# Kernel optimization log

Hardware: AMD Instinct MI355X
Metric: run time of the kernel (lower is better)

Reference implementation:

```python
import jax, jax.numpy as jnp
import numpy as np

EPS = 1e-5
N_HEAD = 12
N_LAYER = 12
D = 768
VOCAB = 50257
SEQ = 1024


def layer_norm(x, w, b):
    m = jnp.mean(x, axis=-1, keepdims=True)
    v = jnp.mean(jnp.square(x - m), axis=-1, keepdims=True)
    return (x - m) * jax.lax.rsqrt(v + EPS) * w + b


def setup_inputs() -> dict:
    key = jax.random.key(0)
    ks = jax.random.split(key, 8)
    s = 0.02  # gpt2 init scale
    return {
        "input_ids": jax.random.randint(ks[0], (SEQ,), 0, VOCAB, dtype=jnp.int64 if jax.config.jax_enable_x64 else jnp.int32),
        "wte": jax.random.normal(ks[1], (VOCAB, D), jnp.float32) * s,
        "wpe": jax.random.normal(ks[2], (SEQ, D), jnp.float32) * s,
        "ln1_w": jnp.ones((N_LAYER, D), jnp.float32),
        "ln1_b": jnp.zeros((N_LAYER, D), jnp.float32),
        "qkv_w": jax.random.normal(ks[3], (N_LAYER, D, 3 * D), jnp.float32) * s,
        "qkv_b": jnp.zeros((N_LAYER, 3 * D), jnp.float32),
        "out_w": jax.random.normal(ks[4], (N_LAYER, D, D), jnp.float32) * s,
        "out_b": jnp.zeros((N_LAYER, D), jnp.float32),
        "ln2_w": jnp.ones((N_LAYER, D), jnp.float32),
        "ln2_b": jnp.zeros((N_LAYER, D), jnp.float32),
        "up_w": jax.random.normal(ks[5], (N_LAYER, D, 4 * D), jnp.float32) * s,
        "up_b": jnp.zeros((N_LAYER, 4 * D), jnp.float32),
        "down_w": jax.random.normal(ks[6], (N_LAYER, 4 * D, D), jnp.float32) * s,
        "down_b": jnp.zeros((N_LAYER, D), jnp.float32),
        "lnf_w": jnp.ones((D,), jnp.float32),
        "lnf_b": jnp.zeros((D,), jnp.float32),
    }


def _attention(x, qkv_w, qkv_b, out_w, out_b, causal_mask):
    S = x.shape[0]
    d = D // N_HEAD
    qkv = x @ qkv_w + qkv_b                  # [S, 3D]
    q, k, v = jnp.split(qkv, 3, axis=-1)     # each [S, D]
    q = q.reshape(S, N_HEAD, d)
    k = k.reshape(S, N_HEAD, d)
    v = v.reshape(S, N_HEAD, d)
    scores = jnp.einsum('shd,thd->hst', q, k) / np.sqrt(d).astype(np.float32)
    scores = jnp.where(causal_mask, scores, jnp.finfo(scores.dtype).min)
    p = jax.nn.softmax(scores, axis=-1)      # [H, S, S]
    o = jnp.einsum('hst,thd->shd', p, v).reshape(S, D)
    return o @ out_w + out_b


def reference(input_ids, wte, wpe, ln1_w, ln1_b, qkv_w, qkv_b, out_w, out_b,
              ln2_w, ln2_b, up_w, up_b, down_w, down_b, lnf_w, lnf_b):
    S = input_ids.shape[0]
    h0 = wte[input_ids] + wpe[jnp.arange(S)]        # [S, D]
    causal_mask = jnp.tril(jnp.ones((S, S), bool))

    layer_params = (ln1_w, ln1_b, qkv_w, qkv_b, out_w, out_b,
                    ln2_w, ln2_b, up_w, up_b, down_w, down_b)

    def step(x, p):
        l1w, l1b, qw, qb, ow, ob, l2w, l2b, uw, ub, dw, db = p
        x = x + _attention(layer_norm(x, l1w, l1b), qw, qb, ow, ob, causal_mask)
        x = x + (jax.nn.gelu(layer_norm(x, l2w, l2b) @ uw + ub, approximate=True) @ dw + db)
        return x, x

    h, ys = jax.lax.scan(step, h0, layer_params)
    layers_output = jnp.concatenate([h0[None], ys], axis=0)   # [L+1, S, D]
    return layer_norm(h, lnf_w, lnf_b), layers_output
```

## Files before the change

kernel.cpp:

```cpp
#include <hip/hip_runtime.h>

typedef __bf16 bf16_t;
typedef __bf16 bf16x8 __attribute__((ext_vector_type(8)));
typedef __bf16 bf16x4 __attribute__((ext_vector_type(4)));
typedef float f32x4 __attribute__((ext_vector_type(4)));

#define MFMA16(a, b, c) __builtin_amdgcn_mfma_f32_16x16x32_bf16(a, b, c, 0, 0, 0)

__device__ __forceinline__ f32x4 zero4() {
    f32x4 z = {0.f, 0.f, 0.f, 0.f};
    return z;
}

__device__ __forceinline__ float gelu_f(float v) {
    float u = 0.7978845608028654f * (v + 0.044715f * v * v * v);
    float e = __expf(2.0f * u);
    float th = 1.0f - 2.0f / (e + 1.0f);
    return 0.5f * v * (1.0f + th);
}

__device__ __forceinline__ void gload16(const bf16_t* g, bf16_t* l) {
    __builtin_amdgcn_global_load_lds((const __attribute__((address_space(1))) void*)g,
                                     (__attribute__((address_space(3))) void*)l, 16, 0, 0);
}

__global__ __launch_bounds__(256) void embed_kernel(const int* __restrict__ ids,
                                                    const float* __restrict__ wte,
                                                    const float* __restrict__ wpe,
                                                    float* __restrict__ x,
                                                    float* __restrict__ out0) {
    const int s = blockIdx.x;
    const int id = ids[s];
    const size_t base = (size_t)s * 768;
#pragma unroll
    for (int r = 0; r < 3; ++r) {
        int d = threadIdx.x + r * 256;
        float v = wte[(size_t)id * 768 + d] + wpe[base + d];
        x[base + d] = v;
        out0[base + d] = v;
    }
}

template <bool BF16OUT>
__global__ __launch_bounds__(256) void ln_kernel(const float* __restrict__ x,
                                                 const float* __restrict__ w,
                                                 const float* __restrict__ b,
                                                 void* __restrict__ outp) {
    const int row = blockIdx.x;
    const int t = threadIdx.x;
    const float* xr = x + (size_t)row * 768;
    float v0 = xr[t], v1 = xr[t + 256], v2 = xr[t + 512];
    float s = v0 + v1 + v2;
    float q = v0 * v0 + v1 * v1 + v2 * v2;
#pragma unroll
    for (int off = 32; off >= 1; off >>= 1) {
        s += __shfl_xor(s, off);
        q += __shfl_xor(q, off);
    }
    __shared__ float sh_s[4], sh_q[4];
    if ((t & 63) == 0) {
        sh_s[t >> 6] = s;
        sh_q[t >> 6] = q;
    }
    __syncthreads();
    s = sh_s[0] + sh_s[1] + sh_s[2] + sh_s[3];
    q = sh_q[0] + sh_q[1] + sh_q[2] + sh_q[3];
    const float mean = s * (1.0f / 768.0f);
    const float var = q * (1.0f / 768.0f) - mean * mean;
    const float rstd = rsqrtf(var + 1e-5f);
    float vv[3] = {v0, v1, v2};
#pragma unroll
    for (int r = 0; r < 3; ++r) {
        int d = t + r * 256;
        float y = (vv[r] - mean) * rstd * w[d] + b[d];
        if (BF16OUT)
            ((bf16_t*)outp)[(size_t)row * 768 + d] = (bf16_t)y;
        else
            ((float*)outp)[(size_t)row * 768 + d] = y;
    }
}

template <bool FINAL>
__global__ __launch_bounds__(256) void ln_reduce(const float* __restrict__ p0,
                                                 const float* __restrict__ p1,
                                                 const float* __restrict__ db,
                                                 float* __restrict__ x,
                                                 float* __restrict__ slice,
                                                 void* __restrict__ lnout,
                                                 const float* __restrict__ w,
                                                 const float* __restrict__ b) {
    const int row = blockIdx.x;
    const int t = threadIdx.x;
    const size_t base = (size_t)row * 768;
    float vv[3];
#pragma unroll
    for (int r = 0; r < 3; ++r) {
        int d = t + r * 256;
        float v = x[base + d] + p0[base + d] + p1[base + d] + db[d];
        vv[r] = v;
        x[base + d] = v;
        slice[base + d] = v;
    }
    float s = vv[0] + vv[1] + vv[2];
    float q = vv[0] * vv[0] + vv[1] * vv[1] + vv[2] * vv[2];
#pragma unroll
    for (int off = 32; off >= 1; off >>= 1) {
        s += __shfl_xor(s, off);
        q += __shfl_xor(q, off);
    }
    __shared__ float sh_s[4], sh_q[4];
    if ((t & 63) == 0) {
        sh_s[t >> 6] = s;
        sh_q[t >> 6] = q;
    }
    __syncthreads();
    s = sh_s[0] + sh_s[1] + sh_s[2] + sh_s[3];
    q = sh_q[0] + sh_q[1] + sh_q[2] + sh_q[3];
    const float mean = s * (1.0f / 768.0f);
    const float var = q * (1.0f / 768.0f) - mean * mean;
    const float rstd = rsqrtf(var + 1e-5f);
#pragma unroll
    for (int r = 0; r < 3; ++r) {
        int d = t + r * 256;
        float y = (vv[r] - mean) * rstd * w[d] + b[d];
        if (FINAL)
            ((float*)lnout)[base + d] = y;
        else
            ((bf16_t*)lnout)[base + d] = (bf16_t)y;
    }
}

__global__ __launch_bounds__(256) void transpose_cvt(const float* __restrict__ src0,
                                                     bf16_t* __restrict__ dst0, int K, int N) {
    const int l = blockIdx.z;
    const float* src = src0 + (size_t)l * K * N;
    bf16_t* dst = dst0 + (size_t)l * N * K;
    const int n0 = blockIdx.x * 32;
    const int k0 = blockIdx.y * 32;
    __shared__ float tile[32][36];
    const int t = threadIdx.x;
    const int r = t >> 3, c4 = (t & 7) * 4;
    const float4 v = *(const float4*)&src[(size_t)(k0 + r) * N + n0 + c4];
    tile[r][c4 + 0] = v.x;
    tile[r][c4 + 1] = v.y;
    tile[r][c4 + 2] = v.z;
    tile[r][c4 + 3] = v.w;
    __syncthreads();
    bf16x4 o;
    o[0] = (bf16_t)tile[c4 + 0][r];
    o[1] = (bf16_t)tile[c4 + 1][r];
    o[2] = (bf16_t)tile[c4 + 2][r];
    o[3] = (bf16_t)tile[c4 + 3][r];
    *(bf16x4*)&dst[(size_t)(n0 + r) * K + k0 + c4] = o;
}

template <int BM, int BN, bool GELU, bool RES>
__global__ __launch_bounds__(256) void gemm3(const bf16_t* __restrict__ A,
                                             const bf16_t* __restrict__ BT,
                                             const float* __restrict__ bias,
                                             const float* __restrict__ res,
                                             float* __restrict__ outF,
                                             bf16_t* __restrict__ outB, int N, int LDK,
                                             int KLEN) {
    constexpr int MW = BM / 32, NW = BN / 32;
    constexpr int TILE = (BM + BN) * 64;
    constexpr int LOADS = (BM + BN) / 32;
    __shared__ __align__(16) bf16_t lds[3 * TILE];
    const int tid = threadIdx.x;
    const int lane = tid & 63, wv = tid >> 6, wm = wv >> 1, wn = wv & 1;
    const int lr = lane & 15, lg = lane >> 4;
    const int m0 = blockIdx.x * BM, n0 = blockIdx.y * BN;
    const bf16_t* Ap = A + (size_t)m0 * LDK + (size_t)blockIdx.z * KLEN;
    const bf16_t* Bp = BT + (size_t)n0 * LDK + (size_t)blockIdx.z * KLEN;

    f32x4 acc[MW][NW];
#pragma unroll
    for (int i = 0; i < MW; ++i)
#pragma unroll
        for (int j = 0; j < NW; ++j) acc[i][j] = zero4();

    const int KT = KLEN >> 6;

    auto stage = [&](int buf, int kt) {
        bf16_t* Ad = lds + buf * TILE;
        bf16_t* Bd = Ad + BM * 64;
#pragma unroll
        for (int i = 0; i < BM / 32; ++i) {
            int v = i * 256 + tid;
            int row = v >> 3, cg = v & 7;
            gload16(Ap + (size_t)row * LDK + kt * 64 + ((cg ^ (row & 7)) << 3), Ad + v * 8);
        }
#pragma unroll
        for (int i = 0; i < BN / 32; ++i) {
            int v = i * 256 + tid;
            int row = v >> 3, cg = v & 7;
            gload16(Bp + (size_t)row * LDK + kt * 64 + ((cg ^ (row & 7)) << 3), Bd + v * 8);
        }
    };

    stage(0, 0);
    stage(1, 1);
    int buf = 0;
    for (int kt = 0; kt < KT; ++kt) {
        if (kt + 1 < KT) {
            if constexpr (LOADS == 4)
                asm volatile("s_waitcnt vmcnt(4)" ::: "memory");
            else
                asm volatile("s_waitcnt vmcnt(3)" ::: "memory");
        } else {
            asm volatile("s_waitcnt vmcnt(0)" ::: "memory");
        }
        __builtin_amdgcn_s_barrier();
        if (kt + 2 < KT) stage((kt + 2) % 3, kt + 2);
        const bf16_t* Ab = lds + buf * TILE;
        const bf16_t* Bb = Ab + BM * 64;
#pragma unroll
        for (int c = 0; c < 2; ++c) {
            bf16x8 af[MW], bfr[NW];
#pragma unroll
            for (int i = 0; i < MW; ++i) {
                int row = wm * (BM / 2) + i * 16 + lr;
                af[i] = *(const bf16x8*)&Ab[row * 64 + ((c * 32 + lg * 8) ^ ((row & 7) << 3))];
            }
#pragma unroll
            for (int j = 0; j < NW; ++j) {
                int row = wn * (BN / 2) + j * 16 + lr;
                bfr[j] = *(const bf16x8*)&Bb[row * 64 + ((c * 32 + lg * 8) ^ ((row & 7) << 3))];
            }
#pragma unroll
            for (int i = 0; i < MW; ++i)
#pragma unroll
                for (int j = 0; j < NW; ++j) acc[i][j] = MFMA16(af[i], bfr[j], acc[i][j]);
        }
        buf = (buf + 1) % 3;
    }

    float* o1 = outF ? outF + (size_t)blockIdx.z * ((size_t)1024 * N) : nullptr;
#pragma unroll
    for (int i = 0; i < MW; ++i) {
#pragma unroll
        for (int j = 0; j < NW; ++j) {
            const int col = n0 + wn * (BN / 2) + j * 16 + lr;
            const float bc = bias ? bias[col] : 0.f;
#pragma unroll
            for (int ii = 0; ii < 4; ++ii) {
                const int rrow = m0 + wm * (BM / 2) + i * 16 + lg * 4 + ii;
                float v = acc[i][j][ii] + bc;
                if (GELU) v = gelu_f(v);
                if (RES) v += res[(size_t)rrow * N + col];
                if (o1) o1[(size_t)rrow * N + col] = v;
                if (outB) outB[(size_t)rrow * N + col] = (bf16_t)v;
            }
        }
    }
}

__global__ __launch_bounds__(256) void attn3_kernel(const bf16_t* __restrict__ qkv,
                                                    bf16_t* __restrict__ out) {
    const int qb = 31 - blockIdx.x;
    const int h = blockIdx.y;
    const int tid = threadIdx.x;
    const int w = tid >> 6, lane = tid & 63;
    const int lr = lane & 15, lg = lane >> 4;
    const int qsub = w & 1, ks = w >> 1;
    const int q0 = qb * 32;
    const int qr0 = q0 + qsub * 16;
    const int NT = (q0 >> 6) + 1;

    __shared__ bf16_t Ksh[2][64][72];
    __shared__ bf16_t Vsh[2][64][72];
    __shared__ bf16_t Ps[4][16][72];
    __shared__ float Osh[2][16][64];
    __shared__ float mlsh[2][2][16];

    bf16x8 aq[2];
    {
        const size_t qoff = (size_t)(qr0 + lr) * 2304 + h * 64;
#pragma unroll
        for (int dt = 0; dt < 2; ++dt) {
            bf16x8 v = *(const bf16x8*)&qkv[qoff + dt * 32 + lg * 8];
#pragma unroll
            for (int i = 0; i < 8; ++i) v[i] = (bf16_t)((float)v[i] * 0.125f);
            aq[dt] = v;
        }
    }

    f32x4 oacc[4];
#pragma unroll
    for (int i = 0; i < 4; ++i) oacc[i] = zero4();
    float mrun[4], lrun[4];
#pragma unroll
    for (int i = 0; i < 4; ++i) {
        mrun[i] = -3.0e38f;
        lrun[i] = 0.f;
    }

    const int st = tid >> 7;
    const int srow = (tid >> 1) & 63;
    const int rounds = (NT + 1) >> 1;

    for (int rr = 0; rr < rounds; ++rr) {
        const int skb = 2 * rr + st;
        if (skb < NT) {
            const int k0s = skb * 64;
#pragma unroll
            for (int s2 = 0; s2 < 2; ++s2) {
                const int dbase = (tid & 1) * 32 + s2 * 16;
                const size_t roff = (size_t)(k0s + srow) * 2304 + h * 64 + dbase;
                bf16x8 ka = *(const bf16x8*)&qkv[roff + 768];
                bf16x8 kbv = *(const bf16x8*)&qkv[roff + 768 + 8];
                bf16x8 va = *(const bf16x8*)&qkv[roff + 1536];
                bf16x8 vb = *(const bf16x8*)&qkv[roff + 1536 + 8];
                *(bf16x8*)&Ksh[st][srow][dbase] = ka;
                *(bf16x8*)&Ksh[st][srow][dbase + 8] = kbv;
#pragma unroll
                for (int i = 0; i < 8; ++i) {
                    Vsh[st][dbase + i][srow] = va[i];
                    Vsh[st][dbase + 8 + i][srow] = vb[i];
                }
            }
        }
        __syncthreads();

        const int kb = 2 * rr + ks;
        if (kb < NT) {
            const int k0 = kb * 64;
            f32x4 sacc[4];
#pragma unroll
            for (int i = 0; i < 4; ++i) sacc[i] = zero4();
#pragma unroll
            for (int kt = 0; kt < 4; ++kt)
#pragma unroll
                for (int dt = 0; dt < 2; ++dt) {
                    bf16x8 bk = *(const bf16x8*)&Ksh[ks][kt * 16 + lr][dt * 32 + lg * 8];
                    sacc[kt] = MFMA16(aq[dt], bk, sacc[kt]);
                }

            if (kb == NT - 1) {
#pragma unroll
                for (int kt = 0; kt < 4; ++kt)
#pragma unroll
                    for (int i = 0; i < 4; ++i)
                        if (k0 + kt * 16 + lr > qr0 + lg * 4 + i) sacc[kt][i] = -3.0e38f;
            }

#pragma unroll
            for (int i = 0; i < 4; ++i) {
                float rmax = fmaxf(fmaxf(sacc[0][i], sacc[1][i]), fmaxf(sacc[2][i], sacc[3][i]));
                rmax = fmaxf(rmax, __shfl_xor(rmax, 1));
                rmax = fmaxf(rmax, __shfl_xor(rmax, 2));
                rmax = fmaxf(rmax, __shfl_xor(rmax, 4));
                rmax = fmaxf(rmax, __shfl_xor(rmax, 8));
                const float mnew = fmaxf(mrun[i], rmax);
                const float sf = __expf(mrun[i] - mnew);
                mrun[i] = mnew;
                float rsum = 0.f;
#pragma unroll
                for (int kt = 0; kt < 4; ++kt) {
                    float p = __expf(sacc[kt][i] - mnew);
                    rsum += p;
                    Ps[w][lg * 4 + i][kt * 16 + lr] = (bf16_t)p;
                }
                rsum += __shfl_xor(rsum, 1);
                rsum += __shfl_xor(rsum, 2);
                rsum += __shfl_xor(rsum, 4);
                rsum += __shfl_xor(rsum, 8);
                lrun[i] = lrun[i] * sf + rsum;
#pragma unroll
                for (int ot = 0; ot < 4; ++ot) oacc[ot][i] *= sf;
            }

            bf16x8 pa0 = *(const bf16x8*)&Ps[w][lr][lg * 8];
            bf16x8 pa1 = *(const bf16x8*)&Ps[w][lr][32 + lg * 8];
#pragma unroll
            for (int ot = 0; ot < 4; ++ot) {
                bf16x8 bv0 = *(const bf16x8*)&Vsh[ks][ot * 16 + lr][lg * 8];
                bf16x8 bv1 = *(const bf16x8*)&Vsh[ks][ot * 16 + lr][32 + lg * 8];
                oacc[ot] = MFMA16(pa0, bv0, oacc[ot]);
                oacc[ot] = MFMA16(pa1, bv1, oacc[ot]);
            }
        }
        __syncthreads();
    }

    if (ks == 1) {
        if (lr == 0) {
#pragma unroll
            for (int i = 0; i < 4; ++i) {
                mlsh[qsub][0][lg * 4 + i] = mrun[i];
                mlsh[qsub][1][lg * 4 + i] = lrun[i];
            }
        }
#pragma unroll
        for (int ot = 0; ot < 4; ++ot)
#pragma unroll
            for (int i = 0; i < 4; ++i) Osh[qsub][lg * 4 + i][ot * 16 + lr] = oacc[ot][i];
    }
    __syncthreads();
    if (ks == 0) {
#pragma unroll
        for (int ot = 0; ot < 4; ++ot)
#pragma unroll
            for (int i = 0; i < 4; ++i) {
                const int row = lg * 4 + i;
                const float m1 = mlsh[qsub][0][row], l1 = mlsh[qsub][1][row];
                const float mm = fmaxf(mrun[i], m1);
                const float fa = __expf(mrun[i] - mm), fb = __expf(m1 - mm);
                const float ll = lrun[i] * fa + l1 * fb;
                const float v = (oacc[ot][i] * fa + Osh[qsub][row][ot * 16 + lr] * fb) / ll;
                out[(size_t)(qr0 + row) * 768 + h * 64 + ot * 16 + lr] = (bf16_t)v;
            }
    }
}

extern "C" void kernel_launch(void* const* d_in, const int* in_sizes, int n_in, void* d_out,
                              int out_size, void* d_ws, size_t ws_size, hipStream_t stream) {
    const int* ids = (const int*)d_in[0];
    const float* wte = (const float*)d_in[1];
    const float* wpe = (const float*)d_in[2];
    const float* ln1_w = (const float*)d_in[3];
    const float* ln1_b = (const float*)d_in[4];
    const float* qkv_w = (const float*)d_in[5];
    const float* qkv_b = (const float*)d_in[6];
    const float* out_w = (const float*)d_in[7];
    const float* out_b = (const float*)d_in[8];
    const float* ln2_w = (const float*)d_in[9];
    const float* ln2_b = (const float*)d_in[10];
    const float* up_w = (const float*)d_in[11];
    const float* up_b = (const float*)d_in[12];
    const float* down_w = (const float*)d_in[13];
    const float* down_b = (const float*)d_in[14];
    const float* lnf_w = (const float*)d_in[15];
    const float* lnf_b = (const float*)d_in[16];

    char* ws = (char*)d_ws;
    float* x = (float*)(ws + 0);
    bf16_t* a_bf = (bf16_t*)(ws + 3145728);
    bf16_t* qkv_bf = (bf16_t*)(ws + 4718592);
    bf16_t* attn_bf = (bf16_t*)(ws + 9437184);
    bf16_t* u_bf = (bf16_t*)(ws + 11010048);
    float* p0 = (float*)(ws + 4718592);
    float* p1 = (float*)(ws + 7864320);
    bf16_t* wqkv_t = (bf16_t*)(ws + 17301504);
    bf16_t* wout_t = (bf16_t*)(ws + 59768832);
    bf16_t* wup_t = (bf16_t*)(ws + 73924608);
    bf16_t* wdown_t = (bf16_t*)(ws + 130547712);

    float* outF = (float*)d_out;
    const size_t SD = (size_t)1024 * 768;
    float* out_layers = outF + SD;

    transpose_cvt<<<dim3(72, 24, 12), 256, 0, stream>>>(qkv_w, wqkv_t, 768, 2304);
    transpose_cvt<<<dim3(24, 24, 12), 256, 0, stream>>>(out_w, wout_t, 768, 768);
    transpose_cvt<<<dim3(96, 24, 12), 256, 0, stream>>>(up_w, wup_t, 768, 3072);
    transpose_cvt<<<dim3(24, 96, 12), 256, 0, stream>>>(down_w, wdown_t, 3072, 768);

    embed_kernel<<<1024, 256, 0, stream>>>(ids, wte, wpe, x, out_layers);

    for (int l = 0; l < 12; ++l) {
        const size_t l768 = (size_t)l * 768;
        if (l == 0)
            ln_kernel<true><<<1024, 256, 0, stream>>>(x, ln1_w, ln1_b, a_bf);
        else
            ln_reduce<false><<<1024, 256, 0, stream>>>(p0, p1, down_b + (l - 1) * 768, x,
                                                       out_layers + (size_t)l * SD, a_bf,
                                                       ln1_w + l768, ln1_b + l768);
        gemm3<64, 64, false, false><<<dim3(16, 36), 256, 0, stream>>>(
            a_bf, wqkv_t + (size_t)l * 2304 * 768, qkv_b + (size_t)l * 2304, nullptr, nullptr,
            qkv_bf, 2304, 768, 768);
        attn3_kernel<<<dim3(32, 12), 256, 0, stream>>>(qkv_bf, attn_bf);
        gemm3<32, 64, false, true><<<dim3(32, 12), 256, 0, stream>>>(
            attn_bf, wout_t + (size_t)l * 768 * 768, out_b + l768, x, x, nullptr, 768, 768,
            768);
        ln_kernel<true><<<1024, 256, 0, stream>>>(x, ln2_w + l768, ln2_b + l768, a_bf);
        gemm3<64, 64, true, false><<<dim3(16, 48), 256, 0, stream>>>(
            a_bf, wup_t + (size_t)l * 3072 * 768, up_b + (size_t)l * 3072, nullptr, nullptr,
            u_bf, 3072, 768, 768);
        gemm3<32, 64, false, false><<<dim3(32, 12, 2), 256, 0, stream>>>(
            u_bf, wdown_t + (size_t)l * 768 * 3072, nullptr, nullptr, p0, nullptr, 768, 3072,
            1536);
    }
    ln_reduce<true><<<1024, 256, 0, stream>>>(p0, p1, down_b + 11 * 768, x,
                                              out_layers + 12 * SD, outF, lnf_w, lnf_b);
}
```

Before: 1.117 ms.

## Emit transposed V from QKV GEMM and async-load swizzled K/V tiles in attention

Measured after the change: 1.085 ms. -2.8%, faster.

```diff
diff --git a/kernel.cpp b/kernel.cpp
--- a/kernel.cpp
+++ b/kernel.cpp
@@ -154,13 +154,14 @@
     *(bf16x4*)&dst[(size_t)(n0 + r) * K + k0 + c4] = o;
 }
 
-template <int BM, int BN, bool GELU, bool RES>
+template <int BM, int BN, bool GELU, bool RES, bool VT>
 __global__ __launch_bounds__(256) void gemm3(const bf16_t* __restrict__ A,
                                              const bf16_t* __restrict__ BT,
                                              const float* __restrict__ bias,
                                              const float* __restrict__ res,
                                              float* __restrict__ outF,
-                                             bf16_t* __restrict__ outB, int N, int LDK,
+                                             bf16_t* __restrict__ outB,
+                                             bf16_t* __restrict__ vt, int N, int LDK,
                                              int KLEN) {
     constexpr int MW = BM / 32, NW = BN / 32;
     constexpr int TILE = (BM + BN) * 64;
@@ -242,6 +243,7 @@
         for (int j = 0; j < NW; ++j) {
             const int col = n0 + wn * (BN / 2) + j * 16 + lr;
             const float bc = bias ? bias[col] : 0.f;
+            float vr[4];
 #pragma unroll
             for (int ii = 0; ii < 4; ++ii) {
                 const int rrow = m0 + wm * (BM / 2) + i * 16 + lg * 4 + ii;
@@ -250,12 +252,21 @@
                 if (RES) v += res[(size_t)rrow * N + col];
                 if (o1) o1[(size_t)rrow * N + col] = v;
                 if (outB) outB[(size_t)rrow * N + col] = (bf16_t)v;
-            }
-        }
-    }
-}
-
-__global__ __launch_bounds__(256) void attn3_kernel(const bf16_t* __restrict__ qkv,
+                vr[ii] = v;
+            }
+            if (VT && col >= 1536) {
+                const int rrow0 = m0 + wm * (BM / 2) + i * 16 + lg * 4;
+                bf16x4 o;
+#pragma unroll
+                for (int ii = 0; ii < 4; ++ii) o[ii] = (bf16_t)vr[ii];
+                *(bf16x4*)&vt[(size_t)(col - 1536) * 1024 + rrow0] = o;
+            }
+        }
+    }
+}
+
+__global__ __launch_bounds__(256) void attn4_kernel(const bf16_t* __restrict__ qkv,
+                                                    const bf16_t* __restrict__ vt,
                                                     bf16_t* __restrict__ out) {
     const int qb = 31 - blockIdx.x;
     const int h = blockIdx.y;
@@ -267,8 +278,8 @@
     const int qr0 = q0 + qsub * 16;
     const int NT = (q0 >> 6) + 1;
 
-    __shared__ bf16_t Ksh[2][64][72];
-    __shared__ bf16_t Vsh[2][64][72];
+    __shared__ __align__(16) bf16_t Ksh[2][64 * 64];
+    __shared__ __align__(16) bf16_t Vsh[2][64 * 64];
     __shared__ bf16_t Ps[4][16][72];
     __shared__ float Osh[2][16][64];
     __shared__ float mlsh[2][2][16];
@@ -295,8 +306,7 @@
         lrun[i] = 0.f;
     }
 
-    const int st = tid >> 7;
-    const int srow = (tid >> 1) & 63;
+    const int st = tid >> 7, tt = tid & 127;
     const int rounds = (NT + 1) >> 1;
 
     for (int rr = 0; rr < rounds; ++rr) {
@@ -304,20 +314,19 @@
         if (skb < NT) {
             const int k0s = skb * 64;
 #pragma unroll
-            for (int s2 = 0; s2 < 2; ++s2) {
-                const int dbase = (tid & 1) * 32 + s2 * 16;
-                const size_t roff = (size_t)(k0s + srow) * 2304 + h * 64 + dbase;
-                bf16x8 ka = *(const bf16x8*)&qkv[roff + 768];
-                bf16x8 kbv = *(const bf16x8*)&qkv[roff + 768 + 8];
-                bf16x8 va = *(const bf16x8*)&qkv[roff + 1536];
-                bf16x8 vb = *(const bf16x8*)&qkv[roff + 1536 + 8];
-                *(bf16x8*)&Ksh[st][srow][dbase] = ka;
-                *(bf16x8*)&Ksh[st][srow][dbase + 8] = kbv;
-#pragma unroll
-                for (int i = 0; i < 8; ++i) {
-                    Vsh[st][dbase + i][srow] = va[i];
-                    Vsh[st][dbase + 8 + i][srow] = vb[i];
-                }
+            for (int i = 0; i < 4; ++i) {
+                int v = i * 128 + tt;
+                int row = v >> 3, cg = v & 7;
+                gload16(qkv + (size_t)(k0s + row) * 2304 + 768 + h * 64 +
+                            ((cg ^ (row & 7)) << 3),
+                        &Ksh[st][v * 8]);
+            }
+#pragma unroll
+            for (int i = 0; i < 4; ++i) {
+                int v = i * 128 + tt;
+                int row = v >> 3, cg = v & 7;
+                gload16(vt + (size_t)(h * 64 + row) * 1024 + k0s + ((cg ^ (row & 7)) << 3),
+                        &Vsh[st][v * 8]);
             }
         }
         __syncthreads();
@@ -329,12 +338,15 @@
 #pragma unroll
             for (int i = 0; i < 4; ++i) sacc[i] = zero4();
 #pragma unroll
-            for (int kt = 0; kt < 4; ++kt)
+            for (int kt = 0; kt < 4; ++kt) {
+                const int row = kt * 16 + lr;
 #pragma unroll
                 for (int dt = 0; dt < 2; ++dt) {
-                    bf16x8 bk = *(const bf16x8*)&Ksh[ks][kt * 16 + lr][dt * 32 + lg * 8];
+                    bf16x8 bk = *(const bf16x8*)&Ksh[ks][row * 64 +
+                                                        ((dt * 32 + lg * 8) ^ ((row & 7) << 3))];
                     sacc[kt] = MFMA16(aq[dt], bk, sacc[kt]);
                 }
+            }
 
             if (kb == NT - 1) {
 #pragma unroll
@@ -374,8 +386,11 @@
             bf16x8 pa1 = *(const bf16x8*)&Ps[w][lr][32 + lg * 8];
 #pragma unroll
             for (int ot = 0; ot < 4; ++ot) {
-                bf16x8 bv0 = *(const bf16x8*)&Vsh[ks][ot * 16 + lr][lg * 8];
-                bf16x8 bv1 = *(const bf16x8*)&Vsh[ks][ot * 16 + lr][32 + lg * 8];
+                const int row = ot * 16 + lr;
+                bf16x8 bv0 = *(const bf16x8*)&Vsh[ks][row * 64 +
+                                                      ((lg * 8) ^ ((row & 7) << 3))];
+                bf16x8 bv1 = *(const bf16x8*)&Vsh[ks][row * 64 +
+                                                      ((32 + lg * 8) ^ ((row & 7) << 3))];
                 oacc[ot] = MFMA16(pa0, bv0, oacc[ot]);
                 oacc[ot] = MFMA16(pa1, bv1, oacc[ot]);
             }
@@ -439,6 +454,7 @@
     bf16_t* qkv_bf = (bf16_t*)(ws + 4718592);
     bf16_t* attn_bf = (bf16_t*)(ws + 9437184);
     bf16_t* u_bf = (bf16_t*)(ws + 11010048);
+    bf16_t* vt = (bf16_t*)(ws + 11010048);
     float* p0 = (float*)(ws + 4718592);
     float* p1 = (float*)(ws + 7864320);
     bf16_t* wqkv_t = (bf16_t*)(ws + 17301504);
@@ -465,20 +481,20 @@
             ln_reduce<false><<<1024, 256, 0, stream>>>(p0, p1, down_b + (l - 1) * 768, x,
                                                        out_layers + (size_t)l * SD, a_bf,
                                                        ln1_w + l768, ln1_b + l768);
-        gemm3<64, 64, false, false><<<dim3(16, 36), 256, 0, stream>>>(
+        gemm3<64, 64, false, false, true><<<dim3(16, 36), 256, 0, stream>>>(
             a_bf, wqkv_t + (size_t)l * 2304 * 768, qkv_b + (size_t)l * 2304, nullptr, nullptr,
-            qkv_bf, 2304, 768, 768);
-        attn3_kernel<<<dim3(32, 12), 256, 0, stream>>>(qkv_bf, attn_bf);
-        gemm3<32, 64, false, true><<<dim3(32, 12), 256, 0, stream>>>(
-            attn_bf, wout_t + (size_t)l * 768 * 768, out_b + l768, x, x, nullptr, 768, 768,
-            768);
+            qkv_bf, vt, 2304, 768, 768);
+        attn4_kernel<<<dim3(32, 12), 256, 0, stream>>>(qkv_bf, vt, attn_bf);
+        gemm3<64, 64, false, true, false><<<dim3(16, 12), 256, 0, stream>>>(
+            attn_bf, wout_t + (size_t)l * 768 * 768, out_b + l768, x, x, nullptr, nullptr, 768,
+            768, 768);
         ln_kernel<true><<<1024, 256, 0, stream>>>(x, ln2_w + l768, ln2_b + l768, a_bf);
-        gemm3<64, 64, true, false><<<dim3(16, 48), 256, 0, stream>>>(
+        gemm3<64, 64, true, false, false><<<dim3(16, 48), 256, 0, stream>>>(
             a_bf, wup_t + (size_t)l * 3072 * 768, up_b + (size_t)l * 3072, nullptr, nullptr,
-            u_bf, 3072, 768, 768);
-        gemm3<32, 64, false, false><<<dim3(32, 12, 2), 256, 0, stream>>>(
-            u_bf, wdown_t + (size_t)l * 768 * 3072, nullptr, nullptr, p0, nullptr, 768, 3072,
-            1536);
+            u_bf, nullptr, 3072, 768, 768);
+        gemm3<64, 64, false, false, false><<<dim3(16, 12, 2), 256, 0, stream>>>(
+            u_bf, wdown_t + (size_t)l * 768 * 3072, nullptr, nullptr, p0, nullptr, nullptr, 768,
+            3072, 1536);
     }
     ln_reduce<true><<<1024, 256, 0, stream>>>(p0, p1, down_b + 11 * 768, x,
                                               out_layers + 12 * SD, outF, lnf_w, lnf_b);
```
